# Kernel tuning notes

Measured on AMD Instinct MI355X. Metric: run time of the kernel, lower is better.

Reference implementation:

```python
import jax, jax.numpy as jnp
import numpy as np

VOCAB_SIZE = 4096
D_EMBED = 256
BETA = 0.25  # unused: module returns raw commit_loss; beta applied by caller


def setup_inputs() -> dict:
    key = jax.random.key(0)
    k_h, k_e = jax.random.split(key)
    h = jax.random.normal(k_h, (16, D_EMBED, 32, 32), dtype=jnp.float32)
    embedding = jax.random.normal(k_e, (VOCAB_SIZE, D_EMBED), dtype=jnp.float32)
    return {"h": h, "embedding": embedding}


def reference(h, embedding):
    B, C, H, W = h.shape
    h = h.astype(jnp.float32)
    # (B, C, H, W) -> (N, C) with N = B*H*W
    h_flat = jnp.transpose(h, (0, 2, 3, 1)).reshape(-1, C)
    dist = (
        jnp.sum(h_flat * h_flat, axis=1, keepdims=True)
        + jnp.sum(embedding * embedding, axis=1)
        - 2.0 * jnp.einsum("nc,vc->nv", h_flat, embedding)
    )
    indices_flat = jnp.argmin(dist, axis=1)
    indices = indices_flat.reshape(B, H, W)
    # gather codebook vectors and restore (B, C, H, W)
    z_q = jnp.transpose(embedding[indices_flat].reshape(B, H, W, C), (0, 3, 1, 2))
    commit_loss = jnp.mean((h - jax.lax.stop_gradient(z_q)) ** 2)
    # straight-through estimator
    z_q_st = h + jax.lax.stop_gradient(z_q - h)
    return z_q_st, indices, commit_loss
```

## Files before the change

### kernel.cpp

```cpp
#include <hip/hip_runtime.h>

#define D 256
#define VOCAB 4096
#define NTOT 16384
#define N_OUT0 4194304

typedef _Float16 half8 __attribute__((ext_vector_type(8)));
typedef float f32x4 __attribute__((ext_vector_type(4)));
typedef unsigned long long u64;

__device__ __forceinline__ u64 pack_key(float d, int v) {
    unsigned u = __float_as_uint(d);
    u ^= ((unsigned)((int)u >> 31)) | 0x80000000u;
    return ((u64)u << 32) | (unsigned)v;
}

__global__ __launch_bounds__(256) void k_pack(const float* __restrict__ h,
                                              const float* __restrict__ emb,
                                              _Float16* __restrict__ Apk,
                                              _Float16* __restrict__ Bpk,
                                              float* __restrict__ hsqp,
                                              float* __restrict__ ht,
                                              float* __restrict__ esq,
                                              float* __restrict__ e2maxp,
                                              float* __restrict__ out2) {
    __shared__ float S[8192];
    const int tid = threadIdx.x;
    const int bid = blockIdx.x;
    if (bid < 512) {
        const int bm = bid >> 3, w = bid & 7;
        const int b = bm >> 2, p0 = (bm & 3) * 256;
        const float* src = h + ((size_t)b << 18) + p0;
#pragma unroll 4
        for (int cl = 0; cl < 32; ++cl)
            S[cl * 256 + tid] = src[(size_t)(w * 32 + cl) << 10 | (unsigned)tid];
        __syncthreads();
        float sq = 0.0f;
#pragma unroll
        for (int cl = 0; cl < 32; ++cl) {
            float t = S[cl * 256 + tid];
            sq = fmaf(t, t, sq);
        }
        hsqp[(size_t)(bm * 8 + w) * 256 + tid] = sq;
        float* htr = ht + ((size_t)(bm * 256 + tid)) * D + w * 32;
#pragma unroll
        for (int c4 = 0; c4 < 8; ++c4) {
            float4 t;
            t.x = S[(c4 * 4 + 0) * 256 + tid];
            t.y = S[(c4 * 4 + 1) * 256 + tid];
            t.z = S[(c4 * 4 + 2) * 256 + tid];
            t.w = S[(c4 * 4 + 3) * 256 + tid];
            *(float4*)(htr + c4 * 4) = t;
        }
        _Float16* dstT = Apk + (size_t)bm * 65536 + (size_t)w * 8192;
#pragma unroll
        for (int i = 0; i < 4; ++i) {
            alignas(16) _Float16 hi[8];
#pragma unroll
            for (int j = 0; j < 8; ++j) hi[j] = (_Float16)S[(i * 8 + j) * 256 + tid];
            *(half8*)(dstT + i * 2048 + tid * 8) = *(half8*)hi;
        }
    } else if (bid < 768) {
        const int bid2 = bid - 512;
        const int bn = bid2 >> 3, w = bid2 & 7;
        const int v0 = bn * 128;
#pragma unroll 4
        for (int i = 0; i < 16; ++i) {
            int flat = i * 256 + tid;
            int r = flat >> 5, cl = flat & 31;
            S[cl * 129 + r] = emb[(size_t)(v0 + r) * D + w * 32 + cl];
        }
        __syncthreads();
        _Float16* dstT = Bpk + (size_t)bn * 32768 + (size_t)w * 4096;
#pragma unroll
        for (int i = 0; i < 2; ++i) {
            int s = i * 256 + tid;
            int q = s >> 7, r = s & 127;
            alignas(16) _Float16 hi[8];
#pragma unroll
            for (int j = 0; j < 8; ++j) hi[j] = (_Float16)S[(q * 8 + j) * 129 + r];
            *(half8*)(dstT + q * 1024 + r * 8) = *(half8*)hi;
        }
    } else {
        __shared__ float sm[4];
        const int pid = bid - 768;
        const int lane = tid & 63, wv = tid >> 6;
        const int v0 = pid * 64;
        float lmax = 0.0f;
#pragma unroll 4
        for (int i = 0; i < 16; ++i) {
            int v = v0 + i * 4 + wv;
            float4 e = *(const float4*)(emb + (size_t)v * D + lane * 4);
            float s = e.x * e.x + e.y * e.y + e.z * e.z + e.w * e.w;
#pragma unroll
            for (int m = 32; m >= 1; m >>= 1) s += __shfl_xor(s, m, 64);
            if (lane == 0) esq[v] = s;
            lmax = fmaxf(lmax, s);
        }
        if (lane == 0) sm[wv] = lmax;
        __syncthreads();
        if (tid == 0) {
            e2maxp[pid] = fmaxf(fmaxf(sm[0], sm[1]), fmaxf(sm[2], sm[3]));
            if (pid == 0) out2[0] = 0.0f;
        }
    }
}

__global__ __launch_bounds__(256, 3) void k_gemm(const _Float16* __restrict__ Apk,
                                                 const _Float16* __restrict__ Bpk,
                                                 const float* __restrict__ esq,
                                                 float2* __restrict__ keys2) {
    __shared__ float2 t2[2048];

    const int tid = threadIdx.x;
    const int bid = blockIdx.x;
    const int swz = (bid & 7) * 512 + (bid >> 3);
    const int bm = swz >> 5, bn = swz & 31;
    const int m0 = bm * 128, n0 = bn * 128;

    const int wv = tid >> 6, l = tid & 63;
    const int wm = wv & 1, wn = wv >> 1;
    const int quad = l >> 4, j16 = l & 15;

    const _Float16* aP = Apk + (size_t)(bm >> 1) * 65536 + (size_t)(bm & 1) * 1024
                       + quad * 2048 + (wm * 64 + j16) * 8;
    const _Float16* bP = Bpk + (size_t)bn * 32768
                       + quad * 1024 + (wn * 64 + j16) * 8;

    f32x4 acc[4][4];
#pragma unroll
    for (int i = 0; i < 4; ++i)
#pragma unroll
        for (int j = 0; j < 4; ++j) acc[i][j] = (f32x4)0.0f;

    half8 af[4], bf[4], afn[4], bfn[4];
#pragma unroll
    for (int mt = 0; mt < 4; ++mt) af[mt] = *(const half8*)(aP + mt * 128);
#pragma unroll
    for (int nt = 0; nt < 4; ++nt) bf[nt] = *(const half8*)(bP + nt * 128);

#pragma unroll
    for (int w = 0; w < 8; ++w) {
        if (w < 7) {
#pragma unroll
            for (int mt = 0; mt < 4; ++mt)
                afn[mt] = *(const half8*)(aP + (w + 1) * 8192 + mt * 128);
#pragma unroll
            for (int nt = 0; nt < 4; ++nt)
                bfn[nt] = *(const half8*)(bP + (w + 1) * 4096 + nt * 128);
        }
        __builtin_amdgcn_s_setprio(1);
#pragma unroll
        for (int mt = 0; mt < 4; ++mt)
#pragma unroll
            for (int nt = 0; nt < 4; ++nt)
                acc[mt][nt] = __builtin_amdgcn_mfma_f32_16x16x32_f16(af[mt], bf[nt], acc[mt][nt], 0, 0, 0);
        __builtin_amdgcn_s_setprio(0);
#pragma unroll
        for (int mt = 0; mt < 4; ++mt) af[mt] = afn[mt];
#pragma unroll
        for (int nt = 0; nt < 4; ++nt) bf[nt] = bfn[nt];
    }

    float es[4];
    unsigned code[4];
#pragma unroll
    for (int nt = 0; nt < 4; ++nt) {
        code[nt] = (unsigned)(wn * 64 + nt * 16 + j16);
        es[nt] = esq[n0 + (int)code[nt]];
    }

    float M1 = __builtin_inff(), M2 = __builtin_inff();
#pragma unroll
    for (int pass = 0; pass < 2; ++pass) {
        if (wn == pass) {
#pragma unroll
            for (int mt = 0; mt < 4; ++mt) {
#pragma unroll
                for (int r = 0; r < 4; ++r) {
                    float c[4];
#pragma unroll
                    for (int nt = 0; nt < 4; ++nt) {
                        float dv = es[nt] - 2.0f * acc[mt][nt][r];
                        c[nt] = __uint_as_float((__float_as_uint(dv) & ~127u) | code[nt]);
                    }
                    float p = fminf(c[0], c[1]), q = fmaxf(c[0], c[1]);
                    float rr = fminf(c[2], c[3]), s = fmaxf(c[2], c[3]);
                    float m1 = fminf(p, rr);
                    float m2 = fminf(fmaxf(p, rr), fminf(q, s));
                    int row = wm * 64 + mt * 16 + quad * 4 + r;
                    t2[row * 16 + (j16 ^ (row & 7))] = make_float2(m1, m2);
                }
            }
        }
        __syncthreads();
        if (tid < 128) {
            const int row = tid;
#pragma unroll
            for (int j = 0; j < 16; ++j) {
                float2 a = t2[row * 16 + (j ^ (row & 7))];
                float t = fmaxf(M1, a.x);
                M1 = fminf(M1, a.x);
                M2 = fminf(fminf(M2, a.y), t);
            }
        }
        __syncthreads();
    }
    if (tid < 128)
        keys2[(size_t)(m0 + tid) * 32 + bn] = make_float2(M1, M2);
}

__device__ __forceinline__ u64 exact_key_ht(const float* __restrict__ ht,
                                            const float* __restrict__ emb,
                                            const float* __restrict__ esq,
                                            int rg, int v, int lane) {
    const float4 h4 = *(const float4*)(ht + (size_t)rg * D + lane * 4);
    const float4 e4 = *(const float4*)(emb + (size_t)v * D + lane * 4);
    float p = h4.x * e4.x;
    p = fmaf(h4.y, e4.y, p);
    p = fmaf(h4.z, e4.z, p);
    p = fmaf(h4.w, e4.w, p);
#pragma unroll
    for (int m = 32; m >= 1; m >>= 1) p += __shfl_xor(p, m, 64);
    return pack_key(esq[v] - 2.0f * p, v);
}

__global__ __launch_bounds__(256) void k_refine(const float* __restrict__ ht,
                                                const float* __restrict__ emb,
                                                const float* __restrict__ esq,
                                                const float* __restrict__ hsqp,
                                                const float* __restrict__ e2maxp,
                                                const float* __restrict__ keys2f,
                                                float* __restrict__ out1) {
    __shared__ float sE2;
    const int tid = threadIdx.x;
    const int lane = tid & 63;
    const int w = tid >> 6;
    const int n0 = blockIdx.x * 32;

    if (tid < 64) {
        float m = e2maxp[tid];
#pragma unroll
        for (int s = 32; s >= 1; s >>= 1) m = fmaxf(m, __shfl_xor(m, s, 64));
        if (tid == 0) sE2 = m;
    }
    __syncthreads();
    const float e2m = sE2;

    int rg = n0 + w * 8;
    float key = keys2f[(size_t)rg * 64 + lane];
#pragma unroll 1
    for (int rr = 0; rr < 8; ++rr, ++rg) {
        float keyn = 0.0f;
        if (rr < 7) keyn = keys2f[(size_t)(rg + 1) * 64 + lane];
        float gm = key;
#pragma unroll
        for (int m = 32; m >= 1; m >>= 1) gm = fminf(gm, __shfl_xor(gm, m, 64));
        float hq = 0.0f;
#pragma unroll
        for (int k = 0; k < 8; ++k) hq += hsqp[(size_t)(rg >> 8) * 2048 + k * 256 + (rg & 255)];
        const float thr = gm + 4.0e-3f * sqrtf(hq * e2m) + 5.0e-2f;
        u64 cmask = __ballot(key <= thr);
        int bidx;
        if (__popcll(cmask) == 1) {
            u64 own = __ballot(key == gm);
            int L = __ffsll((long long)own) - 1;
            bidx = (L >> 1) * 128 + (int)(__float_as_uint(gm) & 127u);
        } else {
            u64 bestk = ~0ULL;
            u64 rescan = 0;
            u64 cm = cmask;
            while (cm) {
                int L = __ffsll((long long)cm) - 1;
                cm &= cm - 1;
                if (L & 1) {
                    rescan |= 1ull << (L >> 1);
                } else {
                    float kL = __shfl(key, L, 64);
                    int v = (L >> 1) * 128 + (int)(__float_as_uint(kL) & 127u);
                    u64 ek = exact_key_ht(ht, emb, esq, rg, v, lane);
                    bestk = ek < bestk ? ek : bestk;
                }
            }
            while (rescan) {
                int bnr = __ffsll((long long)rescan) - 1;
                rescan &= rescan - 1;
                const float* htr = ht + (size_t)rg * D;
                u64 k0 = ~0ULL, k1 = ~0ULL;
#pragma unroll
                for (int c = 0; c < 2; ++c) {
                    int v = bnr * 128 + c * 64 + lane;
                    float p = 0.0f;
#pragma unroll 8
                    for (int d = 0; d < D; d += 4) {
                        float4 hh = *(const float4*)(htr + d);
                        float4 ee = *(const float4*)(emb + (size_t)v * D + d);
                        p = fmaf(hh.x, ee.x, p);
                        p = fmaf(hh.y, ee.y, p);
                        p = fmaf(hh.z, ee.z, p);
                        p = fmaf(hh.w, ee.w, p);
                    }
                    u64 kc = pack_key(esq[v] - 2.0f * p, v);
                    if (c == 0) k0 = kc; else k1 = kc;
                }
                u64 m1 = k0 < k1 ? k0 : k1, m2 = k0 < k1 ? k1 : k0;
#pragma unroll
                for (int m = 32; m >= 1; m >>= 1) {
                    u64 o1 = __shfl_xor(m1, m, 64), o2 = __shfl_xor(m2, m, 64);
                    u64 hi = m1 > o1 ? m1 : o1;
                    m1 = m1 < o1 ? m1 : o1;
                    u64 lo2 = m2 < o2 ? m2 : o2;
                    m2 = hi < lo2 ? hi : lo2;
                }
                u64 e1 = exact_key_ht(ht, emb, esq, rg, (int)(m1 & 0xFFFFFFFFu), lane);
                u64 e2 = exact_key_ht(ht, emb, esq, rg, (int)(m2 & 0xFFFFFFFFu), lane);
                bestk = e1 < bestk ? e1 : bestk;
                bestk = e2 < bestk ? e2 : bestk;
            }
            bidx = (int)(bestk & 0xFFFFFFFFu);
        }
        if (lane == 0) out1[rg] = (float)bidx;
        key = keyn;
    }
}

__global__ __launch_bounds__(256) void k_out(const float* __restrict__ h,
                                             const float* __restrict__ emb,
                                             const float* __restrict__ out1,
                                             float* __restrict__ out0,
                                             float* __restrict__ out2) {
    __shared__ float zq[32][260];
    __shared__ float wred[4];
    const int tid = threadIdx.x;
    const int lane = tid & 63;
    const int w = tid >> 6;
    const int n0 = blockIdx.x * 32;
    const int b = n0 >> 10;
    const int p0 = n0 & 1023;
#pragma unroll
    for (int rr = 0; rr < 8; ++rr) {
        int r = w * 8 + rr;
        unsigned idx = (unsigned)(int)out1[n0 + r];
        float4 e4 = *(const float4*)(emb + (size_t)idx * D + lane * 4);
        *(float4*)&zq[r][lane * 4] = e4;
    }
    __syncthreads();
    float lsum = 0.0f;
    const size_t base = ((size_t)b * D) << 10;
#pragma unroll 4
    for (int it = 0; it < 32; ++it) {
        int c = it * 8 + (tid >> 5);
        int pp = tid & 31;
        float z = zq[pp][c];
        size_t g = base + ((size_t)c << 10) + p0 + pp;
        float hv = h[g];
        out0[g] = hv + (z - hv);
        float d = hv - z;
        lsum = fmaf(d, d, lsum);
    }
#pragma unroll
    for (int m = 32; m >= 1; m >>= 1) lsum += __shfl_xor(lsum, m, 64);
    if (lane == 0) wred[w] = lsum;
    __syncthreads();
    if (tid == 0)
        atomicAdd(out2, (wred[0] + wred[1] + wred[2] + wred[3]) * (1.0f / (float)N_OUT0));
}

extern "C" void kernel_launch(void* const* d_in, const int* in_sizes, int n_in,
                              void* d_out, int out_size, void* d_ws, size_t ws_size,
                              hipStream_t stream) {
    const float* h = (const float*)d_in[0];
    const float* emb = (const float*)d_in[1];
    float* out0 = (float*)d_out;
    float* out1 = out0 + N_OUT0;
    float* out2 = out1 + NTOT;

    char* wsb = (char*)d_ws;
    _Float16* Apk = (_Float16*)wsb;
    _Float16* Bpk = (_Float16*)(wsb + 8388608);
    float* esq = (float*)(wsb + 10485760);
    float* hsqp = (float*)(wsb + 10502144);
    float* e2maxp = (float*)(wsb + 11026432);
    float* keys2f = (float*)(wsb + 11028480);

    hipLaunchKernelGGL(k_pack, dim3(832), dim3(256), 0, stream, h, emb, Apk, Bpk, hsqp, out0, esq, e2maxp, out2);
    hipLaunchKernelGGL(k_gemm, dim3(4096), dim3(256), 0, stream, Apk, Bpk, esq, (float2*)keys2f);
    hipLaunchKernelGGL(k_refine, dim3(NTOT / 32), dim3(256), 0, stream, out0, emb, esq, hsqp, e2maxp, keys2f, out1);
    hipLaunchKernelGGL(k_out, dim3(NTOT / 32), dim3(256), 0, stream, h, emb, out1, out0, out2);
}
```

Baseline: 170.3 us.

## Enlarge GEMM M-tile to 256 and drop transposed h staging buffer

The distance GEMM now computes a 256x128 tile per block (8x4 MFMA accumulators per wave, 2048 blocks, launch bounds lowered to 2 waves per SIMD). This doubles A-fragment reuse of the B tile and halves the per-block key-reduction overhead. Separately, the pack kernel no longer writes a row-major fp32 copy of h into the output buffer. The refine kernel instead reads h directly in its original channel-major layout using strided loads. This removes a 16 MB write from the pack stage, but the refine rescans now make 4 KB-strided uncoalesced accesses, and the larger tile raises register pressure and lowers occupancy.

```diff
diff --git a/kernel.cpp b/kernel.cpp
--- a/kernel.cpp
+++ b/kernel.cpp
@@ -20,7 +20,6 @@
                                               _Float16* __restrict__ Apk,
                                               _Float16* __restrict__ Bpk,
                                               float* __restrict__ hsqp,
-                                              float* __restrict__ ht,
                                               float* __restrict__ esq,
                                               float* __restrict__ e2maxp,
                                               float* __restrict__ out2) {
@@ -42,16 +41,6 @@
             sq = fmaf(t, t, sq);
         }
         hsqp[(size_t)(bm * 8 + w) * 256 + tid] = sq;
-        float* htr = ht + ((size_t)(bm * 256 + tid)) * D + w * 32;
-#pragma unroll
-        for (int c4 = 0; c4 < 8; ++c4) {
-            float4 t;
-            t.x = S[(c4 * 4 + 0) * 256 + tid];
-            t.y = S[(c4 * 4 + 1) * 256 + tid];
-            t.z = S[(c4 * 4 + 2) * 256 + tid];
-            t.w = S[(c4 * 4 + 3) * 256 + tid];
-            *(float4*)(htr + c4 * 4) = t;
-        }
         _Float16* dstT = Apk + (size_t)bm * 65536 + (size_t)w * 8192;
 #pragma unroll
         for (int i = 0; i < 4; ++i) {
@@ -106,36 +95,34 @@
     }
 }
 
-__global__ __launch_bounds__(256, 3) void k_gemm(const _Float16* __restrict__ Apk,
+__global__ __launch_bounds__(256, 2) void k_gemm(const _Float16* __restrict__ Apk,
                                                  const _Float16* __restrict__ Bpk,
                                                  const float* __restrict__ esq,
                                                  float2* __restrict__ keys2) {
-    __shared__ float2 t2[2048];
+    __shared__ float2 t2[4096];
 
     const int tid = threadIdx.x;
     const int bid = blockIdx.x;
-    const int swz = (bid & 7) * 512 + (bid >> 3);
+    const int swz = (bid & 7) * 256 + (bid >> 3);
     const int bm = swz >> 5, bn = swz & 31;
-    const int m0 = bm * 128, n0 = bn * 128;
+    const int m0 = bm * 256, n0 = bn * 128;
 
     const int wv = tid >> 6, l = tid & 63;
     const int wm = wv & 1, wn = wv >> 1;
     const int quad = l >> 4, j16 = l & 15;
 
-    const _Float16* aP = Apk + (size_t)(bm >> 1) * 65536 + (size_t)(bm & 1) * 1024
-                       + quad * 2048 + (wm * 64 + j16) * 8;
-    const _Float16* bP = Bpk + (size_t)bn * 32768
-                       + quad * 1024 + (wn * 64 + j16) * 8;
-
-    f32x4 acc[4][4];
-#pragma unroll
-    for (int i = 0; i < 4; ++i)
+    const _Float16* aP = Apk + (size_t)bm * 65536 + quad * 2048 + (wm * 128 + j16) * 8;
+    const _Float16* bP = Bpk + (size_t)bn * 32768 + quad * 1024 + (wn * 64 + j16) * 8;
+
+    f32x4 acc[8][4];
+#pragma unroll
+    for (int i = 0; i < 8; ++i)
 #pragma unroll
         for (int j = 0; j < 4; ++j) acc[i][j] = (f32x4)0.0f;
 
-    half8 af[4], bf[4], afn[4], bfn[4];
-#pragma unroll
-    for (int mt = 0; mt < 4; ++mt) af[mt] = *(const half8*)(aP + mt * 128);
+    half8 af[8], bf[4], afn[8], bfn[4];
+#pragma unroll
+    for (int mt = 0; mt < 8; ++mt) af[mt] = *(const half8*)(aP + mt * 128);
 #pragma unroll
     for (int nt = 0; nt < 4; ++nt) bf[nt] = *(const half8*)(bP + nt * 128);
 
@@ -143,7 +130,7 @@
     for (int w = 0; w < 8; ++w) {
         if (w < 7) {
 #pragma unroll
-            for (int mt = 0; mt < 4; ++mt)
+            for (int mt = 0; mt < 8; ++mt)
                 afn[mt] = *(const half8*)(aP + (w + 1) * 8192 + mt * 128);
 #pragma unroll
             for (int nt = 0; nt < 4; ++nt)
@@ -151,13 +138,13 @@
         }
         __builtin_amdgcn_s_setprio(1);
 #pragma unroll
-        for (int mt = 0; mt < 4; ++mt)
+        for (int mt = 0; mt < 8; ++mt)
 #pragma unroll
             for (int nt = 0; nt < 4; ++nt)
                 acc[mt][nt] = __builtin_amdgcn_mfma_f32_16x16x32_f16(af[mt], bf[nt], acc[mt][nt], 0, 0, 0);
         __builtin_amdgcn_s_setprio(0);
 #pragma unroll
-        for (int mt = 0; mt < 4; ++mt) af[mt] = afn[mt];
+        for (int mt = 0; mt < 8; ++mt) af[mt] = afn[mt];
 #pragma unroll
         for (int nt = 0; nt < 4; ++nt) bf[nt] = bfn[nt];
     }
@@ -175,7 +162,7 @@
     for (int pass = 0; pass < 2; ++pass) {
         if (wn == pass) {
 #pragma unroll
-            for (int mt = 0; mt < 4; ++mt) {
+            for (int mt = 0; mt < 8; ++mt) {
 #pragma unroll
                 for (int r = 0; r < 4; ++r) {
                     float c[4];
@@ -188,13 +175,13 @@
                     float rr = fminf(c[2], c[3]), s = fmaxf(c[2], c[3]);
                     float m1 = fminf(p, rr);
                     float m2 = fminf(fmaxf(p, rr), fminf(q, s));
-                    int row = wm * 64 + mt * 16 + quad * 4 + r;
+                    int row = wm * 128 + mt * 16 + quad * 4 + r;
                     t2[row * 16 + (j16 ^ (row & 7))] = make_float2(m1, m2);
                 }
             }
         }
         __syncthreads();
-        if (tid < 128) {
+        {
             const int row = tid;
 #pragma unroll
             for (int j = 0; j < 16; ++j) {
@@ -206,26 +193,25 @@
         }
         __syncthreads();
     }
-    if (tid < 128)
-        keys2[(size_t)(m0 + tid) * 32 + bn] = make_float2(M1, M2);
-}
-
-__device__ __forceinline__ u64 exact_key_ht(const float* __restrict__ ht,
-                                            const float* __restrict__ emb,
-                                            const float* __restrict__ esq,
-                                            int rg, int v, int lane) {
-    const float4 h4 = *(const float4*)(ht + (size_t)rg * D + lane * 4);
+    keys2[(size_t)(m0 + tid) * 32 + bn] = make_float2(M1, M2);
+}
+
+__device__ __forceinline__ u64 exact_key_col(const float* __restrict__ h,
+                                             const float* __restrict__ emb,
+                                             const float* __restrict__ esq,
+                                             int rg, int v, int lane) {
+    const float* hB = h + (((size_t)(rg >> 10)) << 18) + (rg & 1023);
     const float4 e4 = *(const float4*)(emb + (size_t)v * D + lane * 4);
-    float p = h4.x * e4.x;
-    p = fmaf(h4.y, e4.y, p);
-    p = fmaf(h4.z, e4.z, p);
-    p = fmaf(h4.w, e4.w, p);
+    float p = hB[(size_t)(lane * 4 + 0) << 10] * e4.x;
+    p = fmaf(hB[(size_t)(lane * 4 + 1) << 10], e4.y, p);
+    p = fmaf(hB[(size_t)(lane * 4 + 2) << 10], e4.z, p);
+    p = fmaf(hB[(size_t)(lane * 4 + 3) << 10], e4.w, p);
 #pragma unroll
     for (int m = 32; m >= 1; m >>= 1) p += __shfl_xor(p, m, 64);
     return pack_key(esq[v] - 2.0f * p, v);
 }
 
-__global__ __launch_bounds__(256) void k_refine(const float* __restrict__ ht,
+__global__ __launch_bounds__(256) void k_refine(const float* __restrict__ h,
                                                 const float* __restrict__ emb,
                                                 const float* __restrict__ esq,
                                                 const float* __restrict__ hsqp,
@@ -278,28 +264,22 @@
                 } else {
                     float kL = __shfl(key, L, 64);
                     int v = (L >> 1) * 128 + (int)(__float_as_uint(kL) & 127u);
-                    u64 ek = exact_key_ht(ht, emb, esq, rg, v, lane);
+                    u64 ek = exact_key_col(h, emb, esq, rg, v, lane);
                     bestk = ek < bestk ? ek : bestk;
                 }
             }
             while (rescan) {
                 int bnr = __ffsll((long long)rescan) - 1;
                 rescan &= rescan - 1;
-                const float* htr = ht + (size_t)rg * D;
+                const float* hB = h + (((size_t)(rg >> 10)) << 18) + (rg & 1023);
                 u64 k0 = ~0ULL, k1 = ~0ULL;
 #pragma unroll
                 for (int c = 0; c < 2; ++c) {
                     int v = bnr * 128 + c * 64 + lane;
                     float p = 0.0f;
 #pragma unroll 8
-                    for (int d = 0; d < D; d += 4) {
-                        float4 hh = *(const float4*)(htr + d);
-                        float4 ee = *(const float4*)(emb + (size_t)v * D + d);
-                        p = fmaf(hh.x, ee.x, p);
-                        p = fmaf(hh.y, ee.y, p);
-                        p = fmaf(hh.z, ee.z, p);
-                        p = fmaf(hh.w, ee.w, p);
-                    }
+                    for (int d = 0; d < D; ++d)
+                        p = fmaf(hB[(size_t)d << 10], emb[(size_t)v * D + d], p);
                     u64 kc = pack_key(esq[v] - 2.0f * p, v);
                     if (c == 0) k0 = kc; else k1 = kc;
                 }
@@ -312,8 +292,8 @@
                     u64 lo2 = m2 < o2 ? m2 : o2;
                     m2 = hi < lo2 ? hi : lo2;
                 }
-                u64 e1 = exact_key_ht(ht, emb, esq, rg, (int)(m1 & 0xFFFFFFFFu), lane);
-                u64 e2 = exact_key_ht(ht, emb, esq, rg, (int)(m2 & 0xFFFFFFFFu), lane);
+                u64 e1 = exact_key_col(h, emb, esq, rg, (int)(m1 & 0xFFFFFFFFu), lane);
+                u64 e2 = exact_key_col(h, emb, esq, rg, (int)(m2 & 0xFFFFFFFFu), lane);
                 bestk = e1 < bestk ? e1 : bestk;
                 bestk = e2 < bestk ? e2 : bestk;
             }
@@ -383,8 +363,8 @@
     float* e2maxp = (float*)(wsb + 11026432);
     float* keys2f = (float*)(wsb + 11028480);
 
-    hipLaunchKernelGGL(k_pack, dim3(832), dim3(256), 0, stream, h, emb, Apk, Bpk, hsqp, out0, esq, e2maxp, out2);
-    hipLaunchKernelGGL(k_gemm, dim3(4096), dim3(256), 0, stream, Apk, Bpk, esq, (float2*)keys2f);
-    hipLaunchKernelGGL(k_refine, dim3(NTOT / 32), dim3(256), 0, stream, out0, emb, esq, hsqp, e2maxp, keys2f, out1);
+    hipLaunchKernelGGL(k_pack, dim3(832), dim3(256), 0, stream, h, emb, Apk, Bpk, hsqp, esq, e2maxp, out2);
+    hipLaunchKernelGGL(k_gemm, dim3(2048), dim3(256), 0, stream, Apk, Bpk, esq, (float2*)keys2f);
+    hipLaunchKernelGGL(k_refine, dim3(NTOT / 32), dim3(256), 0, stream, h, emb, esq, hsqp, e2maxp, keys2f, out1);
     hipLaunchKernelGGL(k_out, dim3(NTOT / 32), dim3(256), 0, stream, h, emb, out1, out0, out2);
 }
```

Result: no change. 173.0 us (+1.6%).
